# Kernel tuning notes

Measured on AMD Instinct MI355X. Metric: run time of the kernel, lower is better.

Reference implementation:

```python
import jax, jax.numpy as jnp
import numpy as np

N_NODES = 100000
N_EDGES = 1600000
NEG_SLOPE = 0.2  # PyG GATConv default


def setup_inputs() -> dict:
    key = jax.random.key(0)
    ks = jax.random.split(key, 10)
    return {
        "x": jax.random.normal(ks[0], (N_NODES, 128), dtype=jnp.float32),
        "edge_index": jax.random.randint(ks[1], (2, N_EDGES), 0, N_NODES, dtype=jnp.int64),
        "W1": jax.random.normal(ks[2], (128, 128), dtype=jnp.float32) * 0.1,
        "a_src1": jax.random.normal(ks[3], (4, 32), dtype=jnp.float32) * 0.1,
        "a_dst1": jax.random.normal(ks[4], (4, 32), dtype=jnp.float32) * 0.1,
        "b1": jax.random.normal(ks[5], (128,), dtype=jnp.float32) * 0.1,
        "W2": jax.random.normal(ks[6], (128, 16), dtype=jnp.float32) * 0.1,
        "a_src2": jax.random.normal(ks[7], (1, 16), dtype=jnp.float32) * 0.1,
        "a_dst2": jax.random.normal(ks[8], (1, 16), dtype=jnp.float32) * 0.1,
        "b2": jax.random.normal(ks[9], (16,), dtype=jnp.float32) * 0.1,
    }


def _gat_layer(x, src, dst, W, a_src, a_dst, b, heads):
    # PyG GATConv (concat=True): xw -> per-edge attention -> segment softmax over
    # incoming edges of each target node -> weighted scatter-sum.
    N = x.shape[0]
    H = heads
    C = W.shape[1] // H
    xw = (x @ W).reshape(N, H, C)                      # [N,H,C]
    al = (xw * a_src).sum(-1)                          # [N,H] source term
    ar = (xw * a_dst).sum(-1)                          # [N,H] target term
    e = jax.nn.leaky_relu(al[src] + ar[dst], NEG_SLOPE)  # [E',H]
    emax = jax.ops.segment_max(e, dst, num_segments=N)   # [N,H]
    em = jnp.exp(e - emax[dst])
    denom = jax.ops.segment_sum(em, dst, num_segments=N)
    alpha = em / denom[dst]                            # [E',H]
    out = jax.ops.segment_sum(xw[src] * alpha[:, :, None], dst, num_segments=N)
    return out.reshape(N, H * C) + b


def reference(x, edge_index, W1, a_src1, a_dst1, b1, W2, a_src2, a_dst2, b2):
    N = x.shape[0]
    loop = jnp.arange(N, dtype=edge_index.dtype)
    # PyG GATConv add_self_loops=True
    src = jnp.concatenate([edge_index[0], loop])
    dst = jnp.concatenate([edge_index[1], loop])
    h = jax.nn.relu(_gat_layer(x, src, dst, W1, a_src1, a_dst1, b1, 4))
    # F.dropout(p=0.5, training=self.training): identity in eval mode
    return _gat_layer(h, src, dst, W2, a_src2, a_dst2, b2, 1)
```

## Files before the change

### kernel.cpp

```cpp
#include <hip/hip_runtime.h>
#include <hip/hip_fp16.h>

#define N_NODES 100000
#define N_EDGES 1600000
#define E_TOT   (N_EDGES + N_NODES)
#define NEG_SLOPE 0.2f
#define PART_EPB 4096
#define BSTRIDE 18432

__global__ __launch_bounds__(256)
void k_part(const int* __restrict__ ei, int* __restrict__ bcnt, int2* __restrict__ pairs) {
    const int t = threadIdx.x;
    const int base = blockIdx.x * PART_EPB;
    __shared__ int lcnt[128];
    __shared__ int lbase[128];
    if (t < 128) lcnt[t] = 0;
    __syncthreads();
    int sr[16], dr[16];
#pragma unroll
    for (int u = 0; u < 16; ++u) {
        const int e = base + u * 256 + t;
        if (e < E_TOT) {
            int s, d;
            if (e < N_EDGES) { s = ei[e]; d = ei[N_EDGES + e]; }
            else             { s = d = e - N_EDGES; }
            sr[u] = s; dr[u] = d;
            atomicAdd(&lcnt[d >> 10], 1);
        } else dr[u] = -1;
    }
    __syncthreads();
    if (t < 128) {
        const int c = lcnt[t];
        lbase[t] = (c > 0) ? atomicAdd(&bcnt[t], c) : 0;
        lcnt[t] = 0;
    }
    __syncthreads();
#pragma unroll
    for (int u = 0; u < 16; ++u) {
        if (dr[u] >= 0) {
            const int bk = dr[u] >> 10;
            const int r = atomicAdd(&lcnt[bk], 1);
            pairs[(size_t)bk * BSTRIDE + lbase[bk] + r] = make_int2(sr[u], dr[u]);
        }
    }
}

__global__ __launch_bounds__(1024)
void k_fill3(const int2* __restrict__ pairs, const int* __restrict__ bcnt,
             int* __restrict__ ioff, int* __restrict__ deg, int* __restrict__ ssrc) {
    const int bucket = blockIdx.x;
    const int t = threadIdx.x;
    const int cnt = bcnt[bucket];
    __shared__ int lhist[1024];
    __shared__ int lcur[1024];
    __shared__ int wsum[16];
    __shared__ int sbase;
    lhist[t] = 0;
    if (t == 0) {
        int b = 0;
        for (int k = 0; k < bucket; ++k) b += bcnt[k];
        sbase = b;
    }
    __syncthreads();
    for (int i = t; i < cnt; i += 1024) {
        const int2 p = pairs[(size_t)bucket * BSTRIDE + i];
        atomicAdd(&lhist[p.y & 1023], 1);
    }
    __syncthreads();
    const int v = lhist[t];
    int inc = v;
    const int lane = t & 63, wid = t >> 6;
#pragma unroll
    for (int o = 1; o < 64; o <<= 1) {
        const int nv = __shfl_up(inc, o, 64);
        if (lane >= o) inc += nv;
    }
    if (lane == 63) wsum[wid] = inc;
    __syncthreads();
    if (t == 0) {
        int acc = 0;
#pragma unroll
        for (int k = 0; k < 16; ++k) { const int tv = wsum[k]; wsum[k] = acc; acc += tv; }
    }
    __syncthreads();
    const int gofs = sbase + (inc - v) + wsum[wid];
    const int d = bucket * 1024 + t;
    if (d < N_NODES) { ioff[d] = gofs; deg[d] = v; }
    lcur[t] = gofs;
    __syncthreads();
    for (int i = t; i < cnt; i += 1024) {
        const int2 p = pairs[(size_t)bucket * BSTRIDE + i];
        const int pos = atomicAdd(&lcur[p.y & 1023], 1);
        ssrc[pos] = p.x;
    }
}

__global__ __launch_bounds__(256)
void k_gemm1(const float* __restrict__ x, const float* __restrict__ W1,
             const float* __restrict__ a_src1, const float* __restrict__ a_dst1,
             __half* __restrict__ xw1h, float* __restrict__ al1, float* __restrict__ ar1) {
    const int t = threadIdx.x;
    const int n0 = blockIdx.x * 32;
    __shared__ float sx[32][128];
    __shared__ float sW[32][128];

    {
        const float4* xg = (const float4*)(x + (size_t)n0 * 128);
#pragma unroll
        for (int i = 0; i < 4; ++i) {
            const int f = t + i * 256;
            ((float4*)sx)[f] = xg[f];
        }
    }

    const int tj = t & 31;
    const int tn = (t >> 5) * 4;
    float4 acc[4] = {{0,0,0,0},{0,0,0,0},{0,0,0,0},{0,0,0,0}};

    for (int kt = 0; kt < 128; kt += 32) {
        __syncthreads();
        const float4* wg = (const float4*)(W1 + (size_t)kt * 128);
#pragma unroll
        for (int i = 0; i < 4; ++i) {
            const int f = t + i * 256;
            ((float4*)sW)[f] = wg[f];
        }
        __syncthreads();
        for (int k = 0; k < 32; k += 4) {
            float4 xv[4];
#pragma unroll
            for (int i = 0; i < 4; ++i)
                xv[i] = *(const float4*)&sx[tn + i][kt + k];
#pragma unroll
            for (int kk = 0; kk < 4; ++kk) {
                const float4 wv = *(const float4*)&sW[k + kk][tj * 4];
#pragma unroll
                for (int i = 0; i < 4; ++i) {
                    const float xs = ((const float*)&xv[i])[kk];
                    acc[i].x = fmaf(xs, wv.x, acc[i].x);
                    acc[i].y = fmaf(xs, wv.y, acc[i].y);
                    acc[i].z = fmaf(xs, wv.z, acc[i].z);
                    acc[i].w = fmaf(xs, wv.w, acc[i].w);
                }
            }
        }
    }

#pragma unroll
    for (int i = 0; i < 4; ++i) {
        __half hp[4];
        hp[0] = __float2half(acc[i].x);
        hp[1] = __float2half(acc[i].y);
        hp[2] = __float2half(acc[i].z);
        hp[3] = __float2half(acc[i].w);
        *(uint2*)&xw1h[(size_t)(n0 + tn + i) * 128 + tj * 4] = *(uint2*)hp;
    }

    const float4 asv = ((const float4*)a_src1)[tj];
    const float4 adv = ((const float4*)a_dst1)[tj];
#pragma unroll
    for (int i = 0; i < 4; ++i) {
        float ps = acc[i].x * asv.x + acc[i].y * asv.y + acc[i].z * asv.z + acc[i].w * asv.w;
        float pd = acc[i].x * adv.x + acc[i].y * adv.y + acc[i].z * adv.z + acc[i].w * adv.w;
#pragma unroll
        for (int o = 1; o < 8; o <<= 1) { ps += __shfl_xor(ps, o, 64); pd += __shfl_xor(pd, o, 64); }
        if ((tj & 7) == 0) {
            const int h = tj >> 3;
            al1[(size_t)(n0 + tn + i) * 4 + h] = ps;
            ar1[(size_t)(n0 + tn + i) * 4 + h] = pd;
        }
    }
}

__global__ __launch_bounds__(256)
void k_aggr1(const int* __restrict__ ssrc, const int* __restrict__ offs,
             const int* __restrict__ deg, const float* __restrict__ al1,
             const float* __restrict__ ar1, const __half* __restrict__ xw1h,
             const float* __restrict__ b1, __half* __restrict__ out1h) {
    const int lane = threadIdx.x & 63;
    const int d = blockIdx.x * 4 + (threadIdx.x >> 6);
    const int g = lane >> 4;
    const int c = lane & 15;
    const int h = c >> 2;
    const int beg = offs[d];
    const int n = deg[d];
    const float arh = ar1[(size_t)d * 4 + h];
    float acc[8] = {0.f, 0.f, 0.f, 0.f, 0.f, 0.f, 0.f, 0.f};
    float dnm = 0.f;

    for (int base = 0; base < n; base += 8) {
#pragma unroll
        for (int u = 0; u < 2; ++u) {
            const int e = base + u * 4 + g;
            const bool p = e < n;
            const int s = ssrc[beg + (p ? e : 0)];
            float v = al1[(size_t)s * 4 + h] + arh;
            v = v > 0.f ? v : NEG_SLOPE * v;
            const float w = p ? __expf(v) : 0.f;
            const uint4 rv = *(const uint4*)&xw1h[(size_t)s * 128 + c * 8];
            const float2 f0 = __half22float2(*(const __half2*)&rv.x);
            const float2 f1 = __half22float2(*(const __half2*)&rv.y);
            const float2 f2 = __half22float2(*(const __half2*)&rv.z);
            const float2 f3 = __half22float2(*(const __half2*)&rv.w);
            acc[0] = fmaf(w, f0.x, acc[0]); acc[1] = fmaf(w, f0.y, acc[1]);
            acc[2] = fmaf(w, f1.x, acc[2]); acc[3] = fmaf(w, f1.y, acc[3]);
            acc[4] = fmaf(w, f2.x, acc[4]); acc[5] = fmaf(w, f2.y, acc[5]);
            acc[6] = fmaf(w, f3.x, acc[6]); acc[7] = fmaf(w, f3.y, acc[7]);
            dnm += w;
        }
    }
#pragma unroll
    for (int i = 0; i < 8; ++i) {
        acc[i] += __shfl_xor(acc[i], 16, 64);
        acc[i] += __shfl_xor(acc[i], 32, 64);
    }
    dnm += __shfl_xor(dnm, 16, 64);
    dnm += __shfl_xor(dnm, 32, 64);
    if (g == 0) {
        const float rc = 1.f / dnm;
        const float4 b01 = *(const float4*)&b1[c * 8];
        const float4 b23 = *(const float4*)&b1[c * 8 + 4];
        const float bb[8] = {b01.x, b01.y, b01.z, b01.w, b23.x, b23.y, b23.z, b23.w};
        __half ho[8];
#pragma unroll
        for (int i = 0; i < 8; ++i) {
            const float hv = acc[i] * rc + bb[i];
            ho[i] = __float2half(hv > 0.f ? hv : 0.f);
        }
        *(uint4*)&out1h[(size_t)d * 128 + c * 8] = *(uint4*)ho;
    }
}

__global__ __launch_bounds__(256)
void k_gemm2(const __half* __restrict__ out1h, const float* __restrict__ W2,
             const float* __restrict__ a_src2, const float* __restrict__ a_dst2,
             __half* __restrict__ xw2h, float* __restrict__ al2, float* __restrict__ ar2) {
    const int t = threadIdx.x;
    const int node0 = blockIdx.x * 16;
    __shared__ float sW[128 * 16];
    __shared__ float sh[16][129];
    for (int i = t; i < 2048; i += 256) sW[i] = W2[i];
    for (int i = t; i < 2048; i += 256) {
        const int nn = i >> 7, kk = i & 127;
        sh[nn][kk] = __half2float(out1h[(size_t)(node0 + nn) * 128 + kk]);
    }
    __syncthreads();
    const int nn = t >> 4;
    const int j = t & 15;
    float acc = 0.f;
#pragma unroll 8
    for (int k = 0; k < 128; ++k)
        acc = fmaf(sh[nn][k], sW[k * 16 + j], acc);
    xw2h[(size_t)(node0 + nn) * 16 + j] = __float2half(acc);

    float ps = acc * a_src2[j];
    float pd = acc * a_dst2[j];
#pragma unroll
    for (int o = 8; o; o >>= 1) { ps += __shfl_xor(ps, o, 64); pd += __shfl_xor(pd, o, 64); }
    if (j == 0) { al2[node0 + nn] = ps; ar2[node0 + nn] = pd; }
}

__global__ __launch_bounds__(256)
void k_aggr2(const int* __restrict__ ssrc, const int* __restrict__ offs,
             const int* __restrict__ deg, const float* __restrict__ al2,
             const float* __restrict__ ar2, const __half* __restrict__ xw2h,
             const float* __restrict__ b2, float* __restrict__ out) {
    const int lane = threadIdx.x & 63;
    const int node = blockIdx.x * 4 + (threadIdx.x >> 6);
    const int j2 = lane & 7;
    const int eL = lane >> 3;
    const int beg = offs[node];
    const int n = deg[node];
    const float ard = ar2[node];
    float a0 = 0.f, a1 = 0.f, dnm = 0.f;
    for (int base = 0; base < n; base += 8) {
        const int e = base + eL;
        const bool p = e < n;
        const int s = ssrc[beg + (p ? e : 0)];
        float v = al2[s] + ard;
        v = v > 0.f ? v : NEG_SLOPE * v;
        const float w = p ? __expf(v) : 0.f;
        const float2 f = __half22float2(*(const __half2*)&xw2h[(size_t)s * 16 + j2 * 2]);
        a0 = fmaf(w, f.x, a0);
        a1 = fmaf(w, f.y, a1);
        dnm += w;
    }
#pragma unroll
    for (int o = 8; o < 64; o <<= 1) {
        a0 += __shfl_xor(a0, o, 64);
        a1 += __shfl_xor(a1, o, 64);
        dnm += __shfl_xor(dnm, o, 64);
    }
    if (eL == 0) {
        out[(size_t)node * 16 + j2 * 2]     = a0 / dnm + b2[j2 * 2];
        out[(size_t)node * 16 + j2 * 2 + 1] = a1 / dnm + b2[j2 * 2 + 1];
    }
}

extern "C" void kernel_launch(void* const* d_in, const int* in_sizes, int n_in,
                              void* d_out, int out_size, void* d_ws, size_t ws_size,
                              hipStream_t stream) {
    const float* x      = (const float*)d_in[0];
    const int*   ei     = (const int*)d_in[1];
    const float* W1     = (const float*)d_in[2];
    const float* a_src1 = (const float*)d_in[3];
    const float* a_dst1 = (const float*)d_in[4];
    const float* b1     = (const float*)d_in[5];
    const float* W2     = (const float*)d_in[6];
    const float* a_src2 = (const float*)d_in[7];
    const float* a_dst2 = (const float*)d_in[8];
    const float* b2     = (const float*)d_in[9];
    float* out = (float*)d_out;

    char* wsb = (char*)d_ws;
    __half* xw1h = (__half*)wsb;
    __half* xw2h = (__half*)wsb;
    float*  al2  = (float*)(wsb + (size_t)N_NODES * 16 * 2);
    float*  ar2  = al2 + N_NODES;
    __half* out1h = (__half*)(wsb + (size_t)N_NODES * 128 * 2);
    int2*   pairs = (int2*)out1h;
    float*  al1  = (float*)(wsb + (size_t)N_NODES * 128 * 4);
    float*  ar1  = al1 + (size_t)N_NODES * 4;
    int* ibcnt = (int*)(ar1 + (size_t)N_NODES * 4);
    int* ioff  = ibcnt + 128;
    int* ideg  = ioff + N_NODES;
    int* isrc  = ideg + N_NODES;

    hipMemsetAsync(ibcnt, 0, 128 * sizeof(int), stream);

    k_part<<<(E_TOT + PART_EPB - 1) / PART_EPB, 256, 0, stream>>>(ei, ibcnt, pairs);
    k_fill3<<<128, 1024, 0, stream>>>(pairs, ibcnt, ioff, ideg, isrc);

    k_gemm1<<<N_NODES / 32, 256, 0, stream>>>(x, W1, a_src1, a_dst1, xw1h, al1, ar1);
    k_aggr1<<<N_NODES / 4, 256, 0, stream>>>(isrc, ioff, ideg, al1, ar1, xw1h, b1, out1h);

    k_gemm2<<<N_NODES / 16, 256, 0, stream>>>(out1h, W2, a_src2, a_dst2, xw2h, al2, ar2);
    k_aggr2<<<N_NODES / 4, 256, 0, stream>>>(isrc, ioff, ideg, al2, ar2, xw2h, b2, out);
}
```

Baseline: 356.7 us.

## Fuse layer-2 projection and attention logits into layer-1 aggregation epilogue

```diff
diff --git a/kernel.cpp b/kernel.cpp
--- a/kernel.cpp
+++ b/kernel.cpp
@@ -176,12 +176,23 @@
 void k_aggr1(const int* __restrict__ ssrc, const int* __restrict__ offs,
              const int* __restrict__ deg, const float* __restrict__ al1,
              const float* __restrict__ ar1, const __half* __restrict__ xw1h,
-             const float* __restrict__ b1, __half* __restrict__ out1h) {
+             const float* __restrict__ b1, const float* __restrict__ W2,
+             const float* __restrict__ a_src2, const float* __restrict__ a_dst2,
+             __half* __restrict__ xw2h, float* __restrict__ al2, float* __restrict__ ar2) {
     const int lane = threadIdx.x & 63;
     const int d = blockIdx.x * 4 + (threadIdx.x >> 6);
     const int g = lane >> 4;
     const int c = lane & 15;
     const int h = c >> 2;
+    float4 w2r[8];
+#pragma unroll
+    for (int i = 0; i < 8; ++i)
+        w2r[i] = *(const float4*)&W2[(8 * c + i) * 16 + 4 * g];
+    const float4 as2 = *(const float4*)&a_src2[4 * g];
+    const float4 ad2 = *(const float4*)&a_dst2[4 * g];
+    const float4 b01 = *(const float4*)&b1[c * 8];
+    const float4 b23 = *(const float4*)&b1[c * 8 + 4];
+
     const int beg = offs[d];
     const int n = deg[d];
     const float arh = ar1[(size_t)d * 4 + h];
@@ -216,48 +227,42 @@
     }
     dnm += __shfl_xor(dnm, 16, 64);
     dnm += __shfl_xor(dnm, 32, 64);
-    if (g == 0) {
-        const float rc = 1.f / dnm;
-        const float4 b01 = *(const float4*)&b1[c * 8];
-        const float4 b23 = *(const float4*)&b1[c * 8 + 4];
-        const float bb[8] = {b01.x, b01.y, b01.z, b01.w, b23.x, b23.y, b23.z, b23.w};
-        __half ho[8];
-#pragma unroll
-        for (int i = 0; i < 8; ++i) {
-            const float hv = acc[i] * rc + bb[i];
-            ho[i] = __float2half(hv > 0.f ? hv : 0.f);
-        }
-        *(uint4*)&out1h[(size_t)d * 128 + c * 8] = *(uint4*)ho;
-    }
-}
-
-__global__ __launch_bounds__(256)
-void k_gemm2(const __half* __restrict__ out1h, const float* __restrict__ W2,
-             const float* __restrict__ a_src2, const float* __restrict__ a_dst2,
-             __half* __restrict__ xw2h, float* __restrict__ al2, float* __restrict__ ar2) {
-    const int t = threadIdx.x;
-    const int node0 = blockIdx.x * 16;
-    __shared__ float sW[128 * 16];
-    __shared__ float sh[16][129];
-    for (int i = t; i < 2048; i += 256) sW[i] = W2[i];
-    for (int i = t; i < 2048; i += 256) {
-        const int nn = i >> 7, kk = i & 127;
-        sh[nn][kk] = __half2float(out1h[(size_t)(node0 + nn) * 128 + kk]);
-    }
-    __syncthreads();
-    const int nn = t >> 4;
-    const int j = t & 15;
-    float acc = 0.f;
-#pragma unroll 8
-    for (int k = 0; k < 128; ++k)
-        acc = fmaf(sh[nn][k], sW[k * 16 + j], acc);
-    xw2h[(size_t)(node0 + nn) * 16 + j] = __float2half(acc);
-
-    float ps = acc * a_src2[j];
-    float pd = acc * a_dst2[j];
-#pragma unroll
-    for (int o = 8; o; o >>= 1) { ps += __shfl_xor(ps, o, 64); pd += __shfl_xor(pd, o, 64); }
-    if (j == 0) { al2[node0 + nn] = ps; ar2[node0 + nn] = pd; }
+
+    const float rc = 1.f / dnm;
+    const float bb[8] = {b01.x, b01.y, b01.z, b01.w, b23.x, b23.y, b23.z, b23.w};
+    float hv[8];
+#pragma unroll
+    for (int i = 0; i < 8; ++i) {
+        const float t = acc[i] * rc + bb[i];
+        hv[i] = t > 0.f ? t : 0.f;
+    }
+
+    float s0 = 0.f, s1 = 0.f, s2 = 0.f, s3 = 0.f;
+#pragma unroll
+    for (int i = 0; i < 8; ++i) {
+        s0 = fmaf(hv[i], w2r[i].x, s0);
+        s1 = fmaf(hv[i], w2r[i].y, s1);
+        s2 = fmaf(hv[i], w2r[i].z, s2);
+        s3 = fmaf(hv[i], w2r[i].w, s3);
+    }
+#pragma unroll
+    for (int o = 1; o < 16; o <<= 1) {
+        s0 += __shfl_xor(s0, o, 64);
+        s1 += __shfl_xor(s1, o, 64);
+        s2 += __shfl_xor(s2, o, 64);
+        s3 += __shfl_xor(s3, o, 64);
+    }
+    if (c == 0) {
+        __half hp[4];
+        hp[0] = __float2half(s0); hp[1] = __float2half(s1);
+        hp[2] = __float2half(s2); hp[3] = __float2half(s3);
+        *(uint2*)&xw2h[(size_t)d * 16 + 4 * g] = *(uint2*)hp;
+    }
+    float ps = s0 * as2.x + s1 * as2.y + s2 * as2.z + s3 * as2.w;
+    float pd = s0 * ad2.x + s1 * ad2.y + s2 * ad2.z + s3 * ad2.w;
+    ps += __shfl_xor(ps, 16, 64); ps += __shfl_xor(ps, 32, 64);
+    pd += __shfl_xor(pd, 16, 64); pd += __shfl_xor(pd, 32, 64);
+    if (lane == 0) { al2[d] = ps; ar2[d] = pd; }
 }
 
 __global__ __launch_bounds__(256)
@@ -314,12 +319,12 @@
 
     char* wsb = (char*)d_ws;
     __half* xw1h = (__half*)wsb;
-    __half* xw2h = (__half*)wsb;
-    float*  al2  = (float*)(wsb + (size_t)N_NODES * 16 * 2);
+    int2*   pairs = (int2*)(wsb + (size_t)N_NODES * 128 * 2);
+    char*   p2 = (char*)(pairs + (size_t)128 * BSTRIDE);
+    __half* xw2h = (__half*)p2;
+    float*  al2  = (float*)(p2 + (size_t)N_NODES * 16 * 2);
     float*  ar2  = al2 + N_NODES;
-    __half* out1h = (__half*)(wsb + (size_t)N_NODES * 128 * 2);
-    int2*   pairs = (int2*)out1h;
-    float*  al1  = (float*)(wsb + (size_t)N_NODES * 128 * 4);
+    float*  al1  = ar2 + N_NODES;
     float*  ar1  = al1 + (size_t)N_NODES * 4;
     int* ibcnt = (int*)(ar1 + (size_t)N_NODES * 4);
     int* ioff  = ibcnt + 128;
@@ -332,8 +337,9 @@
     k_fill3<<<128, 1024, 0, stream>>>(pairs, ibcnt, ioff, ideg, isrc);
 
     k_gemm1<<<N_NODES / 32, 256, 0, stream>>>(x, W1, a_src1, a_dst1, xw1h, al1, ar1);
-    k_aggr1<<<N_NODES / 4, 256, 0, stream>>>(isrc, ioff, ideg, al1, ar1, xw1h, b1, out1h);
-
-    k_gemm2<<<N_NODES / 16, 256, 0, stream>>>(out1h, W2, a_src2, a_dst2, xw2h, al2, ar2);
+
+    k_aggr1<<<N_NODES / 4, 256, 0, stream>>>(isrc, ioff, ideg, al1, ar1, xw1h,
+                                             b1, W2, a_src2, a_dst2, xw2h, al2, ar2);
+
     k_aggr2<<<N_NODES / 4, 256, 0, stream>>>(isrc, ioff, ideg, al2, ar2, xw2h, b2, out);
 }
```

Result: slower. 427.8 us (+19.9%).
